# Kernel tuning notes

Hardware: AMD Instinct MI355X
Metric: run time of the kernel (lower is better)

Reference implementation:

```python
import jax, jax.numpy as jnp
import numpy as np

D_MODEL = 2048
N_HEADS = 16
N_KV_HEADS = 4
HEAD_DIM = D_MODEL // N_HEADS  # 128
WINDOW = 512
SOFTCAP = 50.0
ROPE_THETA = 10000.0
BATCH = 2
SEQ = 2048
NEG_INF = -1e30


def _rope_cos_sin(seq_len, head_dim, theta):
    # inv_freq over half the head dim, duplicated (HF rotate_half convention)
    inv_freq = 1.0 / (theta ** (jnp.arange(0, head_dim, 2, dtype=jnp.float32) / head_dim))
    freqs = jnp.arange(seq_len, dtype=jnp.float32)[:, None] * inv_freq[None, :]  # [S, hd/2]
    emb = jnp.concatenate([freqs, freqs], axis=-1)  # [S, hd]
    return jnp.cos(emb), jnp.sin(emb)


def _rotate_half(x):
    x1, x2 = jnp.split(x, 2, axis=-1)
    return jnp.concatenate([-x2, x1], axis=-1)


def _apply_rope(x, cos, sin):
    # x: [B, S, H, hd]; cos/sin: [S, hd] broadcast over batch & heads (unsqueeze_dim=2)
    c = cos[None, :, None, :]
    s = sin[None, :, None, :]
    return x * c + _rotate_half(x) * s


def setup_inputs() -> dict:
    key = jax.random.key(0)
    ks = jax.random.split(key, 5)
    scale_p = 1.0 / np.sqrt(D_MODEL)
    return {
        "hidden_states": jax.random.normal(ks[0], (BATCH, SEQ, D_MODEL), dtype=jnp.float32),
        "wq": jax.random.normal(ks[1], (N_HEADS * HEAD_DIM, D_MODEL), dtype=jnp.float32) * scale_p,
        "wk": jax.random.normal(ks[2], (N_KV_HEADS * HEAD_DIM, D_MODEL), dtype=jnp.float32) * scale_p,
        "wv": jax.random.normal(ks[3], (N_KV_HEADS * HEAD_DIM, D_MODEL), dtype=jnp.float32) * scale_p,
        "wo": jax.random.normal(ks[4], (D_MODEL, N_HEADS * HEAD_DIM), dtype=jnp.float32) * scale_p,
    }


def reference(hidden_states, wq, wk, wv, wo):
    B, S, _ = hidden_states.shape
    groups = N_HEADS // N_KV_HEADS
    scale = HEAD_DIM ** -0.5

    q = (hidden_states @ wq.T).reshape(B, S, N_HEADS, HEAD_DIM)
    k = (hidden_states @ wk.T).reshape(B, S, N_KV_HEADS, HEAD_DIM)
    v = (hidden_states @ wv.T).reshape(B, S, N_KV_HEADS, HEAD_DIM)

    cos, sin = _rope_cos_sin(S, HEAD_DIM, ROPE_THETA)
    q = _apply_rope(q, cos, sin)
    k = _apply_rope(k, cos, sin)

    # GQA head expansion: each kv head serves `groups` query heads
    k = jnp.repeat(k, groups, axis=2)  # [B, S, H, hd]
    v = jnp.repeat(v, groups, axis=2)

    scores = jnp.einsum("bqhd,bkhd->bhqk", q, k) * scale
    scores = SOFTCAP * jnp.tanh(scores / SOFTCAP)

    i = jnp.arange(S)[:, None]
    j = jnp.arange(S)[None, :]
    allowed = (j <= i) & (j > i - WINDOW)  # causal + sliding window
    scores = jnp.where(allowed[None, None], scores, NEG_INF)

    attn = jax.nn.softmax(scores, axis=-1)
    out = jnp.einsum("bhqk,bkhd->bqhd", attn, v).reshape(B, S, N_HEADS * HEAD_DIM)
    return out @ wo.T
```

## Files before the change

kernel.cpp:

```cpp
#include <hip/hip_runtime.h>
#include <hip/hip_bf16.h>
#include <stdint.h>

#define DM    2048
#define NH    16
#define NKVH  4
#define HD    128
#define WIN   512
#define SEQL  2048
#define BAT   2
#define MR    (BAT*SEQL)
#define NQKV  3072
#define QKSCALE 0.08838834764831845f
#define CAP   50.0f
#define C1F (QKSCALE * 2.0f * 1.4426950408889634f / CAP)
#define C2F (-144.26950408889634f)

typedef unsigned short u16;
typedef __attribute__((ext_vector_type(8))) short short8;
typedef __attribute__((ext_vector_type(4))) float f32x4;
typedef __attribute__((ext_vector_type(16))) float f32x16;

__device__ __forceinline__ u16 f2bf(float f) {
  union { float f; uint32_t u; } v; v.f = f;
  uint32_t r = v.u + 0x7FFFu + ((v.u >> 16) & 1u);
  return (u16)(r >> 16);
}
__device__ __forceinline__ float bf2f(u16 h) {
  union { uint32_t u; float f; } v; v.u = ((uint32_t)h) << 16; return v.f;
}
__device__ __forceinline__ void gld16(const void* g, void* l) {
  __builtin_amdgcn_global_load_lds((const __attribute__((address_space(1))) void*)g,
                                   (__attribute__((address_space(3))) void*)l,
                                   16, 0, 0);
}
__device__ __forceinline__ float exp_softcap(float sv) {
  float t = __builtin_amdgcn_exp2f(sv);
  float u = __builtin_amdgcn_rcpf(t + 1.0f);
  return __builtin_amdgcn_exp2f(u * C2F);
}

__global__ void k_cast(const float* __restrict__ src, u16* __restrict__ dst, int n4) {
  int i = blockIdx.x * 256 + threadIdx.x;
  if (i >= n4) return;
  float4 v = ((const float4*)src)[i];
  ushort4 o;
  o.x = f2bf(v.x); o.y = f2bf(v.y); o.z = f2bf(v.z); o.w = f2bf(v.w);
  ((ushort4*)dst)[i] = o;
}

__global__ void k_rope_table(float* __restrict__ c, float* __restrict__ sn) {
  int s = blockIdx.x, i = threadIdx.x;
  float invf = expf(-(float)i * (9.210340371976184f / 64.0f));
  float a = (float)s * invf;
  c[(s << 6) + i]  = cosf(a);
  sn[(s << 6) + i] = sinf(a);
}

__global__ __launch_bounds__(256, 3) void k_gemm_qkv(const u16* __restrict__ A,
                                                     const u16* __restrict__ Bm,
                                                     u16* __restrict__ qrout,
                                                     u16* __restrict__ krout,
                                                     u16* __restrict__ vtout,
                                                     const float* __restrict__ cosT,
                                                     const float* __restrict__ sinT) {
  __shared__ __align__(16) u16 ldsbuf[2 * 128 * 64];
  u16* ldsA = ldsbuf;
  u16* ldsB = ldsbuf + 128 * 64;
  const int t = threadIdx.x;
  const int K = DM;

  const int nwg  = gridDim.x * gridDim.y;
  const int flat = blockIdx.y * gridDim.x + blockIdx.x;
  const int cpx  = nwg >> 3;
  const int swz  = (flat & 7) * cpx + (flat >> 3);
  const int bn = swz % gridDim.x, bm = swz / gridDim.x;

  const int m0 = bm * 128, n0 = bn * 128;
  const int lane = t & 63, wid = t >> 6;
  const int lr = lane & 15, lk = lane >> 4;
  const int wr = (wid >> 1) * 64, wc = (wid & 1) * 64;
  const int nt = K >> 6;

  const int srow = t >> 3;
  const int scol = (((t & 7) ^ (srow & 7)) << 3);

  f32x4 acc[4][4];
  #pragma unroll
  for (int mi = 0; mi < 4; ++mi)
    #pragma unroll
    for (int ni = 0; ni < 4; ++ni) acc[mi][ni] = f32x4{0.f, 0.f, 0.f, 0.f};

  for (int kt = 0; kt < nt; ++kt) {
    {
      const u16* a0 = A  + (size_t)(m0 + srow) * K + kt * 64 + scol;
      const u16* b0 = Bm + (size_t)(n0 + srow) * K + kt * 64 + scol;
      #pragma unroll
      for (int i = 0; i < 4; ++i) {
        gld16(a0 + (size_t)(i * 32) * K, &ldsA[i * 2048 + t * 8]);
        gld16(b0 + (size_t)(i * 32) * K, &ldsB[i * 2048 + t * 8]);
      }
    }
    __syncthreads();
    #pragma unroll
    for (int ks = 0; ks < 2; ++ks) {
      const int c = ks * 4 + lk;
      short8 af[4], bfv[4];
      #pragma unroll
      for (int mi = 0; mi < 4; ++mi) {
        const int ra = wr + mi * 16 + lr;
        af[mi] = *(const short8*)(ldsA + ra * 64 + ((c ^ (ra & 7)) << 3));
      }
      #pragma unroll
      for (int ni = 0; ni < 4; ++ni) {
        const int rb = wc + ni * 16 + lr;
        bfv[ni] = *(const short8*)(ldsB + rb * 64 + ((c ^ (rb & 7)) << 3));
      }
      #pragma unroll
      for (int mi = 0; mi < 4; ++mi)
        #pragma unroll
        for (int ni = 0; ni < 4; ++ni)
          acc[mi][ni] = __builtin_amdgcn_mfma_f32_16x16x32_bf16(af[mi], bfv[ni], acc[mi][ni], 0, 0, 0);
    }
    if (kt + 1 < nt) __syncthreads();
  }

  __syncthreads();
  const int bb2 = m0 >> 11;

  if (bn < 20) {
    float* exch = (float*)ldsbuf;
    const bool isq = (bn < 16);
    u16* obase = isq ? (qrout + (size_t)(bb2 * NH + bn) * SEQL * HD)
                     : (krout + (size_t)(bb2 * NKVH + (bn - 16)) * SEQL * HD);
    #pragma unroll
    for (int half = 0; half < 2; ++half) {
      #pragma unroll
      for (int mi2 = 0; mi2 < 2; ++mi2)
        #pragma unroll
        for (int ni = 0; ni < 4; ++ni)
          #pragma unroll
          for (int r = 0; r < 4; ++r)
            exch[(wid * 32 + mi2 * 16 + ni * 4 + r) * 64 + lane] = acc[half * 2 + mi2][ni][r];
      __syncthreads();
      #pragma unroll
      for (int mi2 = 0; mi2 < 2; ++mi2) {
        const int mi = half * 2 + mi2;
        const int rbase = m0 + wr + mi * 16 + lk * 4;
        #pragma unroll
        for (int ni = 0; ni < 4; ++ni) {
          const int d64 = ni * 16 + lr;
          const int d   = wc + d64;
          #pragma unroll
          for (int r = 0; r < 4; ++r) {
            const int s = (rbase + r) & (SEQL - 1);
            float x = acc[mi][ni][r];
            float y = exch[((wid ^ 1) * 32 + mi2 * 16 + ni * 4 + r) * 64 + lane];
            float cc = cosT[(s << 6) + d64], ss = sinT[(s << 6) + d64];
            float ov = (wc == 0) ? (x * cc - y * ss) : (x * cc + y * ss);
            if (isq) ov *= C1F;
            obase[(size_t)s * HD + d] = f2bf(ov);
          }
        }
      }
      __syncthreads();
    }
  } else {
    const int kvh = bn - 20;
    u16* vb = vtout + (size_t)(bb2 * NKVH + kvh) * HD * SEQL;
    #pragma unroll
    for (int mi = 0; mi < 4; ++mi) {
      const int s0 = (m0 + wr + mi * 16 + lk * 4) & (SEQL - 1);
      #pragma unroll
      for (int ni = 0; ni < 4; ++ni) {
        const int d = wc + ni * 16 + lr;
        ushort4 w4;
        w4.x = f2bf(acc[mi][ni][0]); w4.y = f2bf(acc[mi][ni][1]);
        w4.z = f2bf(acc[mi][ni][2]); w4.w = f2bf(acc[mi][ni][3]);
        *(ushort4*)(vb + (size_t)d * SEQL + s0) = w4;
      }
    }
  }
}

__global__ __launch_bounds__(512, 4) void k_gemm_ao(const u16* __restrict__ A,
                                                    const u16* __restrict__ Bm,
                                                    float* __restrict__ C,
                                                    int N, int K) {
  __shared__ __align__(16) u16 ldsA[128 * 64];
  __shared__ __align__(16) u16 ldsB[128 * 64];
  const int t = threadIdx.x;

  const int nwg  = gridDim.x * gridDim.y;
  const int flat = blockIdx.y * gridDim.x + blockIdx.x;
  const int cpx  = nwg >> 3;
  const int swz  = (flat & 7) * cpx + (flat >> 3);
  const int bn = swz % gridDim.x, bm = swz / gridDim.x;

  const int m0 = bm * 128, n0 = bn * 128;
  const int lane = t & 63, wid = t >> 6;
  const int lr = lane & 15, lk = lane >> 4;
  const int wr = (wid >> 2) * 64, wc = (wid & 3) * 32;
  const int nt = K >> 6;

  const int srow = t >> 3;
  const int scol = (((t & 7) ^ (srow & 7)) << 3);

  f32x4 acc[4][2];
  #pragma unroll
  for (int mi = 0; mi < 4; ++mi)
    #pragma unroll
    for (int ni = 0; ni < 2; ++ni) acc[mi][ni] = f32x4{0.f, 0.f, 0.f, 0.f};

  for (int kt = 0; kt < nt; ++kt) {
    {
      const u16* a0 = A  + (size_t)(m0 + srow) * K + kt * 64 + scol;
      const u16* b0 = Bm + (size_t)(n0 + srow) * K + kt * 64 + scol;
      #pragma unroll
      for (int i = 0; i < 2; ++i) {
        gld16(a0 + (size_t)(i * 64) * K, &ldsA[i * 4096 + t * 8]);
        gld16(b0 + (size_t)(i * 64) * K, &ldsB[i * 4096 + t * 8]);
      }
    }
    __syncthreads();
    #pragma unroll
    for (int ks = 0; ks < 2; ++ks) {
      const int c = ks * 4 + lk;
      short8 af[4], bfv[2];
      #pragma unroll
      for (int mi = 0; mi < 4; ++mi) {
        const int ra = wr + mi * 16 + lr;
        af[mi] = *(const short8*)(ldsA + ra * 64 + ((c ^ (ra & 7)) << 3));
      }
      #pragma unroll
      for (int ni = 0; ni < 2; ++ni) {
        const int rb = wc + ni * 16 + lr;
        bfv[ni] = *(const short8*)(ldsB + rb * 64 + ((c ^ (rb & 7)) << 3));
      }
      #pragma unroll
      for (int mi = 0; mi < 4; ++mi)
        #pragma unroll
        for (int ni = 0; ni < 2; ++ni)
          acc[mi][ni] = __builtin_amdgcn_mfma_f32_16x16x32_bf16(af[mi], bfv[ni], acc[mi][ni], 0, 0, 0);
    }
    if (kt + 1 < nt) __syncthreads();
  }

  #pragma unroll
  for (int mi = 0; mi < 4; ++mi) {
    #pragma unroll
    for (int ni = 0; ni < 2; ++ni) {
      const int r0 = m0 + wr + mi * 16 + lk * 4;
      const int c  = n0 + wc + ni * 16 + lr;
      #pragma unroll
      for (int r = 0; r < 4; ++r)
        C[(size_t)(r0 + r) * N + c] = acc[mi][ni][r];
    }
  }
}

__global__ __launch_bounds__(256, 2) void k_attn(const u16* __restrict__ qr,
                                                 const u16* __restrict__ kr,
                                                 const u16* __restrict__ vt,
                                                 u16* __restrict__ ao) {
  __shared__ __align__(16) u16 kbuf[2][32 * 128];
  __shared__ __align__(16) u16 vbuf[2][128 * 32];

  const int t = threadIdx.x;
  const int wid = t >> 6, lane = t & 63;
  const int l31 = lane & 31, lh = lane >> 5;
  const int h = blockIdx.x, bq = blockIdx.y, b = blockIdx.z;
  const int kvh = h >> 2;
  const int Q0 = bq * 128;
  const int q0w = Q0 + wid * 32;
  const u16* qb = qr + (size_t)(b * NH + h) * SEQL * HD;
  const u16* kb = kr + (size_t)(b * NKVH + kvh) * SEQL * HD;
  const u16* vb = vt + (size_t)(b * NKVH + kvh) * HD * SEQL;

  short8 qf[8];
  #pragma unroll
  for (int ks = 0; ks < 8; ++ks)
    qf[ks] = *(const short8*)(qb + (size_t)(q0w + l31) * HD + ks * 16 + lh * 8);

  f32x16 o[4];
  #pragma unroll
  for (int dt = 0; dt < 4; ++dt)
    #pragma unroll
    for (int i = 0; i < 16; ++i) o[dt][i] = 0.f;
  float lsum = 0.f;

  int lo = Q0 - (WIN - 1); if (lo < 0) lo = 0;
  const int ktlo = lo >> 5, kthi = (Q0 + 127) >> 5;

  auto stageK = [&](int bufi, int kv0) {
    #pragma unroll
    for (int i = 0; i < 2; ++i) {
      int c = t + i * 256;
      int bb = c << 4;
      int sb = bb ^ (((bb >> 8) & 7) << 4);
      gld16(kb + (size_t)(kv0 + (sb >> 8)) * HD + ((sb & 255) >> 1),
            &kbuf[bufi][c << 3]);
    }
  };
  auto stageV = [&](int bufi, int kv0) {
    #pragma unroll
    for (int i = 0; i < 2; ++i) {
      int c = t + i * 256;
      int bb = c << 4;
      int sb = bb ^ (((bb >> 7) & 3) << 4);
      gld16(vb + (size_t)(sb >> 6) * SEQL + kv0 + ((sb & 63) >> 1),
            &vbuf[bufi][c << 3]);
    }
  };

  stageK(0, ktlo << 5);
  stageV(0, ktlo << 5);
  __syncthreads();

  for (int kt = ktlo; kt <= kthi; ++kt) {
    const int cur = kt & 1;
    if (kt < kthi) { stageK(cur ^ 1, (kt + 1) << 5); stageV(cur ^ 1, (kt + 1) << 5); }
    const int kv0 = kt << 5;
    if (kv0 + 31 >= q0w - (WIN - 1) && kv0 <= q0w + 31) {
      f32x16 sv;
      #pragma unroll
      for (int i = 0; i < 16; ++i) sv[i] = 0.f;
      const u16* lks = kbuf[cur];
      #pragma unroll
      for (int ks = 0; ks < 8; ++ks) {
        int bo = (l31 * 256 + ks * 32 + lh * 16) ^ ((l31 & 7) << 4);
        short8 kf = *(const short8*)(lks + (bo >> 1));
        sv = __builtin_amdgcn_mfma_f32_32x32x16_bf16(kf, qf[ks], sv, 0, 0, 0);
      }
      float p[16];
      const bool interior = (kv0 + 31 <= q0w) && (kv0 >= q0w + 32 - WIN);
      if (interior) {
        #pragma unroll
        for (int r = 0; r < 16; ++r) p[r] = exp_softcap(sv[r]);
      } else {
        const int qg = q0w + l31;
        #pragma unroll
        for (int r = 0; r < 16; ++r) {
          const int kg = kv0 + (r & 3) + 8 * (r >> 2) + 4 * lh;
          float e = exp_softcap(sv[r]);
          p[r] = (kg <= qg && kg > qg - WIN) ? e : 0.f;
        }
      }
      #pragma unroll
      for (int r = 0; r < 16; ++r) lsum += p[r];

      uint32_t w[8];
      #pragma unroll
      for (int r2 = 0; r2 < 8; ++r2) {
        __hip_bfloat162 u = __float22bfloat162_rn(float2{p[2 * r2], p[2 * r2 + 1]});
        w[r2] = *(uint32_t*)&u;
      }
      uint32_t z0 = lh ? w[0] : w[2], z1 = lh ? w[1] : w[3];
      uint32_t z2 = lh ? w[4] : w[6], z3 = lh ? w[5] : w[7];
      uint32_t x0 = __shfl_xor((int)z0, 32), x1 = __shfl_xor((int)z1, 32);
      uint32_t x2 = __shfl_xor((int)z2, 32), x3 = __shfl_xor((int)z3, 32);
      union U8 { uint32_t u[4]; short8 s; };
      U8 pa0, pa1;
      pa0.u[0] = lh ? x0 : w[0];  pa0.u[1] = lh ? x1 : w[1];
      pa0.u[2] = lh ? w[2] : x0;  pa0.u[3] = lh ? w[3] : x1;
      pa1.u[0] = lh ? x2 : w[4];  pa1.u[1] = lh ? x3 : w[5];
      pa1.u[2] = lh ? w[6] : x2;  pa1.u[3] = lh ? w[7] : x3;

      const u16* lvs = vbuf[cur];
      #pragma unroll
      for (int ks2 = 0; ks2 < 2; ++ks2) {
        const short8 paf = ks2 ? pa1.s : pa0.s;
        #pragma unroll
        for (int dt = 0; dt < 4; ++dt) {
          int row = dt * 32 + l31;
          int bo = (row * 64 + ks2 * 32 + lh * 16) ^ (((row >> 1) & 3) << 4);
          short8 vf = *(const short8*)(lvs + (bo >> 1));
          o[dt] = __builtin_amdgcn_mfma_f32_32x32x16_bf16(paf, vf, o[dt], 0, 0, 0);
        }
      }
    }
    __syncthreads();
  }

  lsum += __shfl_xor(lsum, 32);
  float linv = 1.0f / lsum;
  #pragma unroll
  for (int rr = 0; rr < 4; ++rr) {
    #pragma unroll
    for (int r = 0; r < 4; ++r) {
      const int crow = r + 8 * rr + 4 * lh;
      float inv = __shfl(linv, crow);
      const int srow = q0w + crow;
      u16* op = ao + (size_t)(b * SEQL + srow) * DM + h * HD;
      #pragma unroll
      for (int dt = 0; dt < 4; ++dt)
        op[dt * 32 + l31] = f2bf(o[dt][rr * 4 + r] * inv);
    }
  }
}

extern "C" void kernel_launch(void* const* d_in, const int* in_sizes, int n_in,
                              void* d_out, int out_size, void* d_ws, size_t ws_size,
                              hipStream_t stream) {
  (void)in_sizes; (void)n_in; (void)out_size; (void)ws_size;
  const float* hs = (const float*)d_in[0];
  const float* wq = (const float*)d_in[1];
  const float* wk = (const float*)d_in[2];
  const float* wv = (const float*)d_in[3];
  const float* wo = (const float*)d_in[4];
  float* out = (float*)d_out;

  u16* ws    = (u16*)d_ws;
  u16* A_bf  = ws;
  u16* Wqkv  = A_bf + 8388608;
  u16* Wo    = Wqkv + 6291456;
  u16* q_r   = Wo + 4194304;
  u16* k_r   = q_r + 8388608;
  u16* vTb   = k_r + 2097152;
  float* cosT = (float*)(vTb + 2097152);
  float* sinT = cosT + 131072;
  u16* aout = A_bf;

  k_cast<<<8192, 256, 0, stream>>>(hs, A_bf, 2097152);
  k_cast<<<4096, 256, 0, stream>>>(wq, Wqkv, 1048576);
  k_cast<<<1024, 256, 0, stream>>>(wk, Wqkv + 4194304, 262144);
  k_cast<<<1024, 256, 0, stream>>>(wv, Wqkv + 5242880, 262144);
  k_cast<<<4096, 256, 0, stream>>>(wo, Wo, 1048576);
  k_rope_table<<<2048, 64, 0, stream>>>(cosT, sinT);

  k_gemm_qkv<<<dim3(NQKV / 128, MR / 128), 256, 0, stream>>>(A_bf, Wqkv, q_r, k_r, vTb,
                                                             cosT, sinT);

  k_attn<<<dim3(NH, SEQL / 128, BAT), 256, 0, stream>>>(q_r, k_r, vTb, aout);

  k_gemm_ao<<<dim3(DM / 128, MR / 128), 512, 0, stream>>>(aout, Wo, out, DM, DM);
}
```

Before: 174.0 us.

## Fuse prep kernels, remap QKV warps for in-register RoPE, retile output GEMM

Merges the five cast launches and the RoPE table launch into one prep kernel, which removes launch overhead. The QKV GEMM now gives each warp 32 full-width rows, so both RoPE halves sit in the same thread's registers. That drops the LDS exchange and its barriers from the epilogue, at the cost of more B-fragment LDS reads per warp. The output GEMM moves to 128x64 tiles with 256 threads, doubling the grid to improve occupancy and load balance.

```diff
diff --git a/kernel.cpp b/kernel.cpp
--- a/kernel.cpp
+++ b/kernel.cpp
@@ -40,21 +40,34 @@
   return __builtin_amdgcn_exp2f(u * C2F);
 }
 
-__global__ void k_cast(const float* __restrict__ src, u16* __restrict__ dst, int n4) {
-  int i = blockIdx.x * 256 + threadIdx.x;
-  if (i >= n4) return;
-  float4 v = ((const float4*)src)[i];
-  ushort4 o;
-  o.x = f2bf(v.x); o.y = f2bf(v.y); o.z = f2bf(v.z); o.w = f2bf(v.w);
-  ((ushort4*)dst)[i] = o;
-}
-
-__global__ void k_rope_table(float* __restrict__ c, float* __restrict__ sn) {
-  int s = blockIdx.x, i = threadIdx.x;
-  float invf = expf(-(float)i * (9.210340371976184f / 64.0f));
-  float a = (float)s * invf;
-  c[(s << 6) + i]  = cosf(a);
-  sn[(s << 6) + i] = sinf(a);
+__global__ void k_prep(const float* __restrict__ hs, const float* __restrict__ wq,
+                       const float* __restrict__ wk, const float* __restrict__ wv,
+                       const float* __restrict__ wo,
+                       u16* __restrict__ A_bf, u16* __restrict__ Wqkv,
+                       u16* __restrict__ Wo,
+                       float* __restrict__ cosT, float* __restrict__ sinT) {
+  const int bid = blockIdx.x;
+  if (bid < 18432) {
+    const int g = bid * 256 + threadIdx.x;
+    const float* src; u16* dst; int off;
+    if (g < 2097152)      { src = hs; dst = A_bf;           off = 0; }
+    else if (g < 3145728) { src = wq; dst = Wqkv;           off = 2097152; }
+    else if (g < 3407872) { src = wk; dst = Wqkv + 4194304; off = 3145728; }
+    else if (g < 3670016) { src = wv; dst = Wqkv + 5242880; off = 3407872; }
+    else                  { src = wo; dst = Wo;             off = 3670016; }
+    const int li = g - off;
+    float4 v = ((const float4*)src)[li];
+    ushort4 o;
+    o.x = f2bf(v.x); o.y = f2bf(v.y); o.z = f2bf(v.z); o.w = f2bf(v.w);
+    ((ushort4*)dst)[li] = o;
+  } else {
+    const int rt = (bid - 18432) * 256 + threadIdx.x;
+    const int s = rt >> 6, i = rt & 63;
+    float invf = expf(-(float)i * (9.210340371976184f / 64.0f));
+    float a = (float)s * invf;
+    cosT[rt] = cosf(a);
+    sinT[rt] = sinf(a);
+  }
 }
 
 __global__ __launch_bounds__(256, 3) void k_gemm_qkv(const u16* __restrict__ A,
@@ -64,9 +77,8 @@
                                                      u16* __restrict__ vtout,
                                                      const float* __restrict__ cosT,
                                                      const float* __restrict__ sinT) {
-  __shared__ __align__(16) u16 ldsbuf[2 * 128 * 64];
-  u16* ldsA = ldsbuf;
-  u16* ldsB = ldsbuf + 128 * 64;
+  __shared__ __align__(16) u16 ldsA[128 * 64];
+  __shared__ __align__(16) u16 ldsB[128 * 64];
   const int t = threadIdx.x;
   const int K = DM;
 
@@ -79,22 +91,23 @@
   const int m0 = bm * 128, n0 = bn * 128;
   const int lane = t & 63, wid = t >> 6;
   const int lr = lane & 15, lk = lane >> 4;
-  const int wr = (wid >> 1) * 64, wc = (wid & 1) * 64;
+  const int wr = wid * 32;
   const int nt = K >> 6;
+  (void)n0;
 
   const int srow = t >> 3;
   const int scol = (((t & 7) ^ (srow & 7)) << 3);
 
-  f32x4 acc[4][4];
-  #pragma unroll
-  for (int mi = 0; mi < 4; ++mi)
-    #pragma unroll
-    for (int ni = 0; ni < 4; ++ni) acc[mi][ni] = f32x4{0.f, 0.f, 0.f, 0.f};
+  f32x4 acc[2][8];
+  #pragma unroll
+  for (int mi = 0; mi < 2; ++mi)
+    #pragma unroll
+    for (int ni = 0; ni < 8; ++ni) acc[mi][ni] = f32x4{0.f, 0.f, 0.f, 0.f};
 
   for (int kt = 0; kt < nt; ++kt) {
     {
       const u16* a0 = A  + (size_t)(m0 + srow) * K + kt * 64 + scol;
-      const u16* b0 = Bm + (size_t)(n0 + srow) * K + kt * 64 + scol;
+      const u16* b0 = Bm + (size_t)(bn * 128 + srow) * K + kt * 64 + scol;
       #pragma unroll
       for (int i = 0; i < 4; ++i) {
         gld16(a0 + (size_t)(i * 32) * K, &ldsA[i * 2048 + t * 8]);
@@ -105,75 +118,61 @@
     #pragma unroll
     for (int ks = 0; ks < 2; ++ks) {
       const int c = ks * 4 + lk;
-      short8 af[4], bfv[4];
-      #pragma unroll
-      for (int mi = 0; mi < 4; ++mi) {
+      short8 af[2], bfv[8];
+      #pragma unroll
+      for (int mi = 0; mi < 2; ++mi) {
         const int ra = wr + mi * 16 + lr;
         af[mi] = *(const short8*)(ldsA + ra * 64 + ((c ^ (ra & 7)) << 3));
       }
       #pragma unroll
-      for (int ni = 0; ni < 4; ++ni) {
-        const int rb = wc + ni * 16 + lr;
+      for (int ni = 0; ni < 8; ++ni) {
+        const int rb = ni * 16 + lr;
         bfv[ni] = *(const short8*)(ldsB + rb * 64 + ((c ^ (rb & 7)) << 3));
       }
       #pragma unroll
-      for (int mi = 0; mi < 4; ++mi)
-        #pragma unroll
-        for (int ni = 0; ni < 4; ++ni)
+      for (int mi = 0; mi < 2; ++mi)
+        #pragma unroll
+        for (int ni = 0; ni < 8; ++ni)
           acc[mi][ni] = __builtin_amdgcn_mfma_f32_16x16x32_bf16(af[mi], bfv[ni], acc[mi][ni], 0, 0, 0);
     }
     if (kt + 1 < nt) __syncthreads();
   }
 
-  __syncthreads();
   const int bb2 = m0 >> 11;
 
   if (bn < 20) {
-    float* exch = (float*)ldsbuf;
     const bool isq = (bn < 16);
     u16* obase = isq ? (qrout + (size_t)(bb2 * NH + bn) * SEQL * HD)
                      : (krout + (size_t)(bb2 * NKVH + (bn - 16)) * SEQL * HD);
     #pragma unroll
-    for (int half = 0; half < 2; ++half) {
-      #pragma unroll
-      for (int mi2 = 0; mi2 < 2; ++mi2)
-        #pragma unroll
-        for (int ni = 0; ni < 4; ++ni)
-          #pragma unroll
-          for (int r = 0; r < 4; ++r)
-            exch[(wid * 32 + mi2 * 16 + ni * 4 + r) * 64 + lane] = acc[half * 2 + mi2][ni][r];
-      __syncthreads();
-      #pragma unroll
-      for (int mi2 = 0; mi2 < 2; ++mi2) {
-        const int mi = half * 2 + mi2;
-        const int rbase = m0 + wr + mi * 16 + lk * 4;
-        #pragma unroll
-        for (int ni = 0; ni < 4; ++ni) {
-          const int d64 = ni * 16 + lr;
-          const int d   = wc + d64;
-          #pragma unroll
-          for (int r = 0; r < 4; ++r) {
-            const int s = (rbase + r) & (SEQL - 1);
-            float x = acc[mi][ni][r];
-            float y = exch[((wid ^ 1) * 32 + mi2 * 16 + ni * 4 + r) * 64 + lane];
-            float cc = cosT[(s << 6) + d64], ss = sinT[(s << 6) + d64];
-            float ov = (wc == 0) ? (x * cc - y * ss) : (x * cc + y * ss);
-            if (isq) ov *= C1F;
-            obase[(size_t)s * HD + d] = f2bf(ov);
-          }
+    for (int mi = 0; mi < 2; ++mi) {
+      const int rbase = m0 + wr + mi * 16 + lk * 4;
+      #pragma unroll
+      for (int ni = 0; ni < 4; ++ni) {
+        const int d64 = ni * 16 + lr;
+        #pragma unroll
+        for (int r = 0; r < 4; ++r) {
+          const int s = (rbase + r) & (SEQL - 1);
+          float x = acc[mi][ni][r];
+          float y = acc[mi][ni + 4][r];
+          float cc = cosT[(s << 6) + d64], ss = sinT[(s << 6) + d64];
+          float o0 = x * cc - y * ss;
+          float o1 = y * cc + x * ss;
+          if (isq) { o0 *= C1F; o1 *= C1F; }
+          obase[(size_t)s * HD + d64]      = f2bf(o0);
+          obase[(size_t)s * HD + d64 + 64] = f2bf(o1);
         }
       }
-      __syncthreads();
     }
   } else {
     const int kvh = bn - 20;
     u16* vb = vtout + (size_t)(bb2 * NKVH + kvh) * HD * SEQL;
     #pragma unroll
-    for (int mi = 0; mi < 4; ++mi) {
+    for (int mi = 0; mi < 2; ++mi) {
       const int s0 = (m0 + wr + mi * 16 + lk * 4) & (SEQL - 1);
       #pragma unroll
-      for (int ni = 0; ni < 4; ++ni) {
-        const int d = wc + ni * 16 + lr;
+      for (int ni = 0; ni < 8; ++ni) {
+        const int d = ni * 16 + lr;
         ushort4 w4;
         w4.x = f2bf(acc[mi][ni][0]); w4.y = f2bf(acc[mi][ni][1]);
         w4.z = f2bf(acc[mi][ni][2]); w4.w = f2bf(acc[mi][ni][3]);
@@ -183,12 +182,12 @@
   }
 }
 
-__global__ __launch_bounds__(512, 4) void k_gemm_ao(const u16* __restrict__ A,
+__global__ __launch_bounds__(256, 4) void k_gemm_ao(const u16* __restrict__ A,
                                                     const u16* __restrict__ Bm,
                                                     float* __restrict__ C,
                                                     int N, int K) {
   __shared__ __align__(16) u16 ldsA[128 * 64];
-  __shared__ __align__(16) u16 ldsB[128 * 64];
+  __shared__ __align__(16) u16 ldsB[64 * 64];
   const int t = threadIdx.x;
 
   const int nwg  = gridDim.x * gridDim.y;
@@ -197,10 +196,10 @@
   const int swz  = (flat & 7) * cpx + (flat >> 3);
   const int bn = swz % gridDim.x, bm = swz / gridDim.x;
 
-  const int m0 = bm * 128, n0 = bn * 128;
+  const int m0 = bm * 128, n0 = bn * 64;
   const int lane = t & 63, wid = t >> 6;
   const int lr = lane & 15, lk = lane >> 4;
-  const int wr = (wid >> 2) * 64, wc = (wid & 3) * 32;
+  const int wr = (wid >> 1) * 64, wc = (wid & 1) * 32;
   const int nt = K >> 6;
 
   const int srow = t >> 3;
@@ -217,10 +216,11 @@
       const u16* a0 = A  + (size_t)(m0 + srow) * K + kt * 64 + scol;
       const u16* b0 = Bm + (size_t)(n0 + srow) * K + kt * 64 + scol;
       #pragma unroll
-      for (int i = 0; i < 2; ++i) {
-        gld16(a0 + (size_t)(i * 64) * K, &ldsA[i * 4096 + t * 8]);
-        gld16(b0 + (size_t)(i * 64) * K, &ldsB[i * 4096 + t * 8]);
-      }
+      for (int i = 0; i < 4; ++i)
+        gld16(a0 + (size_t)(i * 32) * K, &ldsA[i * 2048 + t * 8]);
+      #pragma unroll
+      for (int i = 0; i < 2; ++i)
+        gld16(b0 + (size_t)(i * 32) * K, &ldsB[i * 2048 + t * 8]);
     }
     __syncthreads();
     #pragma unroll
@@ -421,17 +421,12 @@
   float* sinT = cosT + 131072;
   u16* aout = A_bf;
 
-  k_cast<<<8192, 256, 0, stream>>>(hs, A_bf, 2097152);
-  k_cast<<<4096, 256, 0, stream>>>(wq, Wqkv, 1048576);
-  k_cast<<<1024, 256, 0, stream>>>(wk, Wqkv + 4194304, 262144);
-  k_cast<<<1024, 256, 0, stream>>>(wv, Wqkv + 5242880, 262144);
-  k_cast<<<4096, 256, 0, stream>>>(wo, Wo, 1048576);
-  k_rope_table<<<2048, 64, 0, stream>>>(cosT, sinT);
+  k_prep<<<18944, 256, 0, stream>>>(hs, wq, wk, wv, wo, A_bf, Wqkv, Wo, cosT, sinT);
 
   k_gemm_qkv<<<dim3(NQKV / 128, MR / 128), 256, 0, stream>>>(A_bf, Wqkv, q_r, k_r, vTb,
                                                              cosT, sinT);
 
   k_attn<<<dim3(NH, SEQL / 128, BAT), 256, 0, stream>>>(q_r, k_r, vTb, aout);
 
-  k_gemm_ao<<<dim3(DM / 128, MR / 128), 512, 0, stream>>>(aout, Wo, out, DM, DM);
-}
+  k_gemm_ao<<<dim3(DM / 64, MR / 128), 256, 0, stream>>>(aout, Wo, out, DM, DM);
+}
```

Result: faster. 164.0 us (-5.7%).
